# Optimization experiments

Hardware: AMD Instinct MI355X
Metric: run time of the kernel (lower is better)

The kernel has to match this reference:

```python
import jax, jax.numpy as jnp
import numpy as np

HEAD_DIM = 64
CLIP = 64  # clipping_distance
B, S = 32, 1024


def setup_inputs() -> dict:
    key = jax.random.key(0)
    kq, kk, kv, km, kt = jax.random.split(key, 5)
    q = jax.random.normal(kq, (B, S, HEAD_DIM), dtype=jnp.float32)
    k = jax.random.normal(kk, (B, S, HEAD_DIM), dtype=jnp.float32)
    v = jax.random.normal(kv, (B, S, HEAD_DIM), dtype=jnp.float32)
    mask = jax.random.randint(km, (B, S, S), 0, 2).astype(jnp.bool_)
    pos_table = jax.random.normal(kt, (2 * CLIP + 1, HEAD_DIM), dtype=jnp.float32)
    return {"q": q, "k": k, "v": v, "mask": mask, "pos_table": pos_table}


def reference(q, k, v, mask, pos_table):
    scaling = 1.0 / np.sqrt(HEAD_DIM).astype(np.float32)
    Sq, Sk = q.shape[1], k.shape[1]
    # relative positions k_idx - q_idx, clipped to [-CLIP, CLIP]
    rel = jnp.arange(Sk)[None, :] - jnp.arange(Sq)[:, None]      # [Sq, Sk]
    idx = jnp.clip(rel, -CLIP, CLIP) + CLIP                      # [Sq, Sk]
    pe = pos_table[idx]                                          # [Sq, Sk, D]
    # content logits + relative positional logits
    logits = jnp.einsum('bqd,bkd->bqk', q, k) + jnp.einsum('bqd,qkd->bqk', q, pe)
    logits = logits * scaling
    logits = jnp.where(mask, -jnp.inf, logits)
    attn = jax.nn.softmax(logits, axis=-1)                       # [B, Sq, Sk]
    return jnp.einsum('bqk,bkd->bqd', attn, v)
```

## Files before the change

### kernel.cpp

```cpp
#include <hip/hip_runtime.h>
#include <stdint.h>

#define BATCH 32
#define SEQ   1024
#define DIM   64
#define NKT   (SEQ / 64)

typedef uint8_t  u8;
typedef uint16_t u16;
typedef uint32_t u32;
typedef unsigned long long u64;
typedef __attribute__((ext_vector_type(8))) __bf16 bf16x8;
typedef __attribute__((ext_vector_type(4))) float  f32x4;
typedef __attribute__((ext_vector_type(4))) u32    u32x4;

__device__ __forceinline__ float fexp2(float x) {
#if __has_builtin(__builtin_amdgcn_exp2f)
    return __builtin_amdgcn_exp2f(x);
#else
    return exp2f(x);
#endif
}

__device__ __forceinline__ u16 f2bf(float f) {
    u32 x = __builtin_bit_cast(u32, f);
    x += 0x7FFFu + ((x >> 16) & 1u);
    return (u16)(x >> 16);
}

__device__ __forceinline__ bf16x8 cvt8(const float* __restrict__ p) {
    f32x4 a = *reinterpret_cast<const f32x4*>(p);
    f32x4 b = *reinterpret_cast<const f32x4*>(p + 4);
    u16 t[8];
    t[0] = f2bf(a[0]); t[1] = f2bf(a[1]); t[2] = f2bf(a[2]); t[3] = f2bf(a[3]);
    t[4] = f2bf(b[0]); t[5] = f2bf(b[1]); t[6] = f2bf(b[2]); t[7] = f2bf(b[3]);
    return __builtin_bit_cast(bf16x8, *reinterpret_cast<u32x4*>(t));
}

__device__ __forceinline__ bf16x8 cvt8s(const float* __restrict__ p, float s) {
    f32x4 a = *reinterpret_cast<const f32x4*>(p);
    f32x4 b = *reinterpret_cast<const f32x4*>(p + 4);
    u16 t[8];
    t[0] = f2bf(a[0] * s); t[1] = f2bf(a[1] * s); t[2] = f2bf(a[2] * s); t[3] = f2bf(a[3] * s);
    t[4] = f2bf(b[0] * s); t[5] = f2bf(b[1] * s); t[6] = f2bf(b[2] * s); t[7] = f2bf(b[3] * s);
    return __builtin_bit_cast(bf16x8, *reinterpret_cast<u32x4*>(t));
}

__device__ __forceinline__ bf16x8 ldg8(const u16* p) {
    u32x4 u = *reinterpret_cast<const u32x4*>(p);
    return __builtin_bit_cast(bf16x8, u);
}

__device__ __forceinline__ u32 pack4(u32x4 a) {
    return (u32)(a[0] != 0) | ((u32)(a[1] != 0) << 8) |
           ((u32)(a[2] != 0) << 16) | ((u32)(a[3] != 0) << 24);
}

__global__ __launch_bounds__(256) void prep_kv(
    const float* __restrict__ kg, const float* __restrict__ vg,
    u16* __restrict__ kb, u16* __restrict__ vtb_) {
    __shared__ u16 tile[64][72];
    const int t  = threadIdx.x;
    const int b  = blockIdx.x >> 4;
    const int k0 = (blockIdx.x & 15) * 64;

    {
        int kk = t >> 2;
        int d0 = (t & 3) * 16;
        const float* src = kg + ((size_t)b * SEQ + k0 + kk) * DIM + d0;
        u16 tmp[16];
#pragma unroll
        for (int i = 0; i < 4; ++i) {
            f32x4 a = *reinterpret_cast<const f32x4*>(src + i * 4);
            tmp[i * 4 + 0] = f2bf(a[0]); tmp[i * 4 + 1] = f2bf(a[1]);
            tmp[i * 4 + 2] = f2bf(a[2]); tmp[i * 4 + 3] = f2bf(a[3]);
        }
        u16* dst = kb + ((size_t)b * SEQ + k0 + kk) * DIM + d0;
        *reinterpret_cast<u32x4*>(dst)     = *reinterpret_cast<u32x4*>(tmp);
        *reinterpret_cast<u32x4*>(dst + 8) = *reinterpret_cast<u32x4*>(tmp + 8);
    }
    {
        const float* vb = vg + (size_t)b * SEQ * DIM;
        int kk = t >> 2;
        int d0 = (t & 3) * 16;
        const float* src = vb + (size_t)(k0 + kk) * DIM + d0;
        u16 tmp[16];
#pragma unroll
        for (int i = 0; i < 4; ++i) {
            f32x4 a = *reinterpret_cast<const f32x4*>(src + i * 4);
            tmp[i * 4 + 0] = f2bf(a[0]); tmp[i * 4 + 1] = f2bf(a[1]);
            tmp[i * 4 + 2] = f2bf(a[2]); tmp[i * 4 + 3] = f2bf(a[3]);
        }
        *reinterpret_cast<u32x4*>(&tile[kk][d0])     = *reinterpret_cast<u32x4*>(tmp);
        *reinterpret_cast<u32x4*>(&tile[kk][d0 + 8]) = *reinterpret_cast<u32x4*>(tmp + 8);
    }
    __syncthreads();
    u16* vtb = vtb_ + (size_t)b * DIM * SEQ;
#pragma unroll
    for (int i = 0; i < 2; ++i) {
        int d  = t / 8 + i * 32;
        int ks = (t % 8) * 8;
        u16 tmp[8];
#pragma unroll
        for (int j = 0; j < 8; ++j) tmp[j] = tile[ks + j][d];
        *reinterpret_cast<u32x4*>(vtb + (size_t)d * SEQ + k0 + ks) =
            *reinterpret_cast<u32x4*>(tmp);
    }
}

__global__ __launch_bounds__(512, 2) void attn_fast9(
    const float* __restrict__ qg, const u16* __restrict__ kbf,
    const u16* __restrict__ vt, const int* __restrict__ maskg,
    const float* __restrict__ ptg, float* __restrict__ outg) {
    __shared__ float qp[64][132];
    __shared__ u16   plds[8][16][72];
    __shared__ u8    mlds[8][16][64];

    const int b    = blockIdx.y;
    const int q0   = blockIdx.x * 64;
    const int tid  = threadIdx.x;
    const int wave = tid >> 6;
    const int lane = tid & 63;
    const int wq   = wave & 3;
    const int wk   = wave >> 2;
    const int quad = lane >> 4;
    const int c16  = lane & 15;

    const float SC = 0.125f * 1.44269504088896340736f;

    const float* qb = qg + ((size_t)b * SEQ + q0) * DIM;

    const bf16x8 qA0 = cvt8s(qb + (size_t)(wq * 16 + c16) * DIM + quad * 8, SC);
    const bf16x8 qA1 = cvt8s(qb + (size_t)(wq * 16 + c16) * DIM + 32 + quad * 8, SC);

    {
        const int jt0 = wk ? 5 : 0, jt1 = wk ? 9 : 5;
        for (int jt = jt0; jt < jt1; ++jt) {
            int j0 = jt * 16;
            int jr = min(j0 + c16, 128);
            bf16x8 b0 = cvt8(ptg + (size_t)jr * DIM + quad * 8);
            bf16x8 b1 = cvt8(ptg + (size_t)jr * DIM + 32 + quad * 8);
            f32x4 acc = {0.f, 0.f, 0.f, 0.f};
            acc = __builtin_amdgcn_mfma_f32_16x16x32_bf16(qA0, b0, acc, 0, 0, 0);
            acc = __builtin_amdgcn_mfma_f32_16x16x32_bf16(qA1, b1, acc, 0, 0, 0);
            int jcol = j0 + c16;
            if (jcol <= 128) {
#pragma unroll
                for (int r = 0; r < 4; ++r)
                    qp[wq * 16 + quad * 4 + r][jcol] = acc[r];
            }
        }
    }
    __syncthreads();

    float cL[4], cR[4];
#pragma unroll
    for (int r = 0; r < 4; ++r) {
        cL[r] = qp[wq * 16 + quad * 4 + r][0];
        cR[r] = qp[wq * 16 + quad * 4 + r][128];
    }

    const u16* kb_base  = kbf + (size_t)b * SEQ * DIM;
    const u16* vtb_base = vt  + (size_t)b * DIM * SEQ;
    const int  row_min  = q0 + wq * 16;
    const int  ktbase   = wk * 8;

    const int* mrow = maskg + ((size_t)b * SEQ + q0 + wq * 16 + (lane >> 2)) * SEQ +
                      (lane & 3) * 16;

    u32x4 mreg[2][4];
#pragma unroll
    for (int s = 0; s < 2; ++s) {
        const int* p = mrow + (size_t)(ktbase + s) * 64;
        mreg[s][0] = *reinterpret_cast<const u32x4*>(p);
        mreg[s][1] = *reinterpret_cast<const u32x4*>(p + 4);
        mreg[s][2] = *reinterpret_cast<const u32x4*>(p + 8);
        mreg[s][3] = *reinterpret_cast<const u32x4*>(p + 12);
    }

    bf16x8 kc0[4], kc1[4];
#pragma unroll
    for (int sub = 0; sub < 4; ++sub) {
        const u16* kr = kb_base + (size_t)(ktbase * 64 + sub * 16 + c16) * DIM;
        kc0[sub] = ldg8(kr + quad * 8);
        kc1[sub] = ldg8(kr + 32 + quad * 8);
    }

    float l_part[4];
    f32x4 O[4];
#pragma unroll
    for (int r = 0; r < 4; ++r) l_part[r] = 0.f;
#pragma unroll
    for (int d = 0; d < 4; ++d) O[d] = f32x4{0.f, 0.f, 0.f, 0.f};

#pragma unroll
    for (int j = 0; j < 8; ++j) {
        const int kt = ktbase + j;
        const int k0 = kt * 64;
        const int ms = j & 1;

        {
            u32x4 pk;
            pk[0] = pack4(mreg[ms][0]); pk[1] = pack4(mreg[ms][1]);
            pk[2] = pack4(mreg[ms][2]); pk[3] = pack4(mreg[ms][3]);
            *reinterpret_cast<u32x4*>(&mlds[wave][lane >> 2][(lane & 3) * 16]) = pk;
        }
        {
            const int* p = mrow + (size_t)((kt + 2) & 15) * 64;
            mreg[ms][0] = *reinterpret_cast<const u32x4*>(p);
            mreg[ms][1] = *reinterpret_cast<const u32x4*>(p + 4);
            mreg[ms][2] = *reinterpret_cast<const u32x4*>(p + 8);
            mreg[ms][3] = *reinterpret_cast<const u32x4*>(p + 12);
        }

        f32x4 S[4];
        __builtin_amdgcn_s_setprio(1);
#pragma unroll
        for (int sub = 0; sub < 4; ++sub) {
            f32x4 acc = {0.f, 0.f, 0.f, 0.f};
            acc = __builtin_amdgcn_mfma_f32_16x16x32_bf16(qA0, kc0[sub], acc, 0, 0, 0);
            acc = __builtin_amdgcn_mfma_f32_16x16x32_bf16(qA1, kc1[sub], acc, 0, 0, 0);
            S[sub] = acc;
        }
        __builtin_amdgcn_s_setprio(0);

        {
            const int kn = (ktbase + ((j + 1) & 7)) * 64;
#pragma unroll
            for (int sub = 0; sub < 4; ++sub) {
                const u16* kr = kb_base + (size_t)(kn + sub * 16 + c16) * DIM;
                kc0[sub] = ldg8(kr + quad * 8);
                kc1[sub] = ldg8(kr + 32 + quad * 8);
            }
        }

        bf16x8 vf0[4], vf1[4];
#pragma unroll
        for (int d = 0; d < 4; ++d) {
            const u16* vr = vtb_base + (size_t)(d * 16 + c16) * SEQ + k0;
            vf0[d] = ldg8(vr + quad * 8);
            vf1[d] = ldg8(vr + 32 + quad * 8);
        }

        const bool farL = (k0 + 127 <= row_min);
        const bool farR = (k0 >= row_min + 79);

        if (farL | farR) {
#pragma unroll
            for (int r = 0; r < 4; ++r) {
                const int row_l = quad * 4 + r;
                const float c = farL ? cL[r] : cR[r];
                float rs = 0.f;
#pragma unroll
                for (int sub = 0; sub < 4; ++sub) {
                    u8 mv = mlds[wave][row_l][sub * 16 + c16];
                    float e = mv ? 0.f : fexp2(S[sub][r] + c);
                    rs += e;
                    plds[wave][row_l][sub * 16 + c16] = f2bf(e);
                }
                l_part[r] += rs;
            }
        } else {
#pragma unroll
            for (int r = 0; r < 4; ++r) {
                const int row_l = quad * 4 + r;
                const int row_g = row_min + row_l;
                float rs = 0.f;
#pragma unroll
                for (int sub = 0; sub < 4; ++sub) {
                    int col_g = k0 + sub * 16 + c16;
                    int rel = col_g - row_g;
                    rel = rel < -64 ? -64 : (rel > 64 ? 64 : rel);
                    float x = S[sub][r] + qp[wq * 16 + row_l][rel + 64];
                    u8 mv = mlds[wave][row_l][sub * 16 + c16];
                    float e = mv ? 0.f : fexp2(x);
                    rs += e;
                    plds[wave][row_l][sub * 16 + c16] = f2bf(e);
                }
                l_part[r] += rs;
            }
        }

        bf16x8 pA0 = *reinterpret_cast<bf16x8*>(&plds[wave][c16][quad * 8]);
        bf16x8 pA1 = *reinterpret_cast<bf16x8*>(&plds[wave][c16][32 + quad * 8]);
        __builtin_amdgcn_s_setprio(1);
#pragma unroll
        for (int d = 0; d < 4; ++d) {
            O[d] = __builtin_amdgcn_mfma_f32_16x16x32_bf16(pA0, vf0[d], O[d], 0, 0, 0);
            O[d] = __builtin_amdgcn_mfma_f32_16x16x32_bf16(pA1, vf1[d], O[d], 0, 0, 0);
        }
        __builtin_amdgcn_s_setprio(0);
    }

    float l_run[4];
#pragma unroll
    for (int r = 0; r < 4; ++r) {
        float rs = l_part[r];
        rs += __shfl_xor(rs, 1);
        rs += __shfl_xor(rs, 2);
        rs += __shfl_xor(rs, 4);
        rs += __shfl_xor(rs, 8);
        l_run[r] = rs;
    }

    __syncthreads();
    float* cmb = &qp[0][0];
    const int cbase = (wq * 64 + lane) * 24;
    if (wk == 1) {
#pragma unroll
        for (int r = 0; r < 4; ++r) cmb[cbase + r] = l_run[r];
#pragma unroll
        for (int d = 0; d < 4; ++d)
#pragma unroll
            for (int r = 0; r < 4; ++r)
                cmb[cbase + 4 + d * 4 + r] = O[d][r];
    }
    __syncthreads();
    if (wk == 0) {
        float* ob = outg + ((size_t)b * SEQ + q0) * DIM;
#pragma unroll
        for (int r = 0; r < 4; ++r) {
            float inv = 1.f / (l_run[r] + cmb[cbase + r]);
            int row_l = wq * 16 + quad * 4 + r;
#pragma unroll
            for (int d = 0; d < 4; ++d) {
                float o = O[d][r] + cmb[cbase + 4 + d * 4 + r];
                ob[(size_t)row_l * DIM + d * 16 + c16] = o * inv;
            }
        }
    }
}

__global__ __launch_bounds__(256) void vt_kernel(const float* __restrict__ v,
                                                 u16* __restrict__ vt) {
    __shared__ u16 tile[64][72];
    const int b  = blockIdx.y;
    const int k0 = blockIdx.x * 64;
    const int t  = threadIdx.x;
    const float* vb  = v  + (size_t)b * SEQ * DIM;
    u16*         vtb = vt + (size_t)b * DIM * SEQ;

    {
        int kk = t >> 2;
        int d0 = (t & 3) * 16;
        const float* src = vb + (size_t)(k0 + kk) * DIM + d0;
        u16 tmp[16];
#pragma unroll
        for (int i = 0; i < 4; ++i) {
            f32x4 a = *reinterpret_cast<const f32x4*>(src + i * 4);
            tmp[i * 4 + 0] = f2bf(a[0]); tmp[i * 4 + 1] = f2bf(a[1]);
            tmp[i * 4 + 2] = f2bf(a[2]); tmp[i * 4 + 3] = f2bf(a[3]);
        }
        *reinterpret_cast<u32x4*>(&tile[kk][d0])     = *reinterpret_cast<u32x4*>(tmp);
        *reinterpret_cast<u32x4*>(&tile[kk][d0 + 8]) = *reinterpret_cast<u32x4*>(tmp + 8);
    }
    __syncthreads();
#pragma unroll
    for (int i = 0; i < 2; ++i) {
        int d  = t / 8 + i * 32;
        int ks = (t % 8) * 8;
        u16 tmp[8];
#pragma unroll
        for (int j = 0; j < 8; ++j) tmp[j] = tile[ks + j][d];
        *reinterpret_cast<u32x4*>(vtb + (size_t)d * SEQ + k0 + ks) =
            *reinterpret_cast<u32x4*>(tmp);
    }
}

template <bool USE_VT>
__global__ __launch_bounds__(256, 2) void attn_kernel(
    const float* __restrict__ qg, const float* __restrict__ kg,
    const void* __restrict__ vgv, const int* __restrict__ maskg,
    const float* __restrict__ ptg, float* __restrict__ outg) {
    __shared__ float qp[64][132];
    __shared__ int   mlds[4][16][68];
    __shared__ u16   plds[4][16][72];

    const int b    = blockIdx.y;
    const int q0   = blockIdx.x * 64;
    const int tid  = threadIdx.x;
    const int wave = tid >> 6;
    const int lane = tid & 63;
    const int quad = lane >> 4;
    const int c16  = lane & 15;

    const float* qb = qg + ((size_t)b * SEQ + q0) * DIM;
    const float* kb = kg + (size_t)b * SEQ * DIM;
    const int*   mb = maskg + ((size_t)b * SEQ + q0) * SEQ;

    const bf16x8 qA0 = cvt8(qb + (size_t)(wave * 16 + c16) * DIM + quad * 8);
    const bf16x8 qA1 = cvt8(qb + (size_t)(wave * 16 + c16) * DIM + 32 + quad * 8);

    for (int jt = 0; jt < 9; ++jt) {
        int j0 = jt * 16;
        int jr = min(j0 + c16, 128);
        bf16x8 b0 = cvt8(ptg + (size_t)jr * DIM + quad * 8);
        bf16x8 b1 = cvt8(ptg + (size_t)jr * DIM + 32 + quad * 8);
        f32x4 acc = {0.f, 0.f, 0.f, 0.f};
        acc = __builtin_amdgcn_mfma_f32_16x16x32_bf16(qA0, b0, acc, 0, 0, 0);
        acc = __builtin_amdgcn_mfma_f32_16x16x32_bf16(qA1, b1, acc, 0, 0, 0);
        int jcol = j0 + c16;
        if (jcol <= 128) {
#pragma unroll
            for (int r = 0; r < 4; ++r)
                qp[wave * 16 + quad * 4 + r][jcol] = acc[r];
        }
    }

    float m_run[4], l_run[4];
    f32x4 O[4];
#pragma unroll
    for (int r = 0; r < 4; ++r) { m_run[r] = -1e30f; l_run[r] = 0.f; }
#pragma unroll
    for (int d = 0; d < 4; ++d) O[d] = f32x4{0.f, 0.f, 0.f, 0.f};

#pragma unroll 1
    for (int kt = 0; kt < NKT; ++kt) {
        const int k0 = kt * 64;
        {
            int row_l = lane >> 2;
            const int* mrow = mb + (size_t)(wave * 16 + row_l) * SEQ + k0;
#pragma unroll
            for (int i = 0; i < 4; ++i) {
                int seg = (lane & 3) + i * 4;
                *reinterpret_cast<u32x4*>(&mlds[wave][row_l][seg * 4]) =
                    *reinterpret_cast<const u32x4*>(mrow + seg * 4);
            }
        }

        f32x4 S[4];
#pragma unroll
        for (int sub = 0; sub < 4; ++sub) {
            const float* kr = kb + (size_t)(k0 + sub * 16 + c16) * DIM;
            bf16x8 kb0 = cvt8(kr + quad * 8);
            bf16x8 kb1 = cvt8(kr + 32 + quad * 8);
            f32x4 acc = {0.f, 0.f, 0.f, 0.f};
            acc = __builtin_amdgcn_mfma_f32_16x16x32_bf16(qA0, kb0, acc, 0, 0, 0);
            acc = __builtin_amdgcn_mfma_f32_16x16x32_bf16(qA1, kb1, acc, 0, 0, 0);
            S[sub] = acc;
        }

        float sv[4][4];
#pragma unroll
        for (int sub = 0; sub < 4; ++sub) {
#pragma unroll
            for (int r = 0; r < 4; ++r) {
                int row_l = quad * 4 + r;
                int row_g = q0 + wave * 16 + row_l;
                int col_g = k0 + sub * 16 + c16;
                int rel = col_g - row_g;
                rel = rel < -64 ? -64 : (rel > 64 ? 64 : rel);
                float x = (S[sub][r] + qp[wave * 16 + row_l][rel + 64]) * 0.125f;
                int mv = mlds[wave][row_l][sub * 16 + c16];
                sv[sub][r] = mv ? -1e30f : x;
            }
        }

        float m_new[4], alpha[4];
#pragma unroll
        for (int r = 0; r < 4; ++r) {
            float rmax = fmaxf(fmaxf(sv[0][r], sv[1][r]), fmaxf(sv[2][r], sv[3][r]));
            rmax = fmaxf(rmax, __shfl_xor(rmax, 1));
            rmax = fmaxf(rmax, __shfl_xor(rmax, 2));
            rmax = fmaxf(rmax, __shfl_xor(rmax, 4));
            rmax = fmaxf(rmax, __shfl_xor(rmax, 8));
            m_new[r] = fmaxf(m_run[r], rmax);
            alpha[r] = __expf(m_run[r] - m_new[r]);
            m_run[r] = m_new[r];
        }
#pragma unroll
        for (int r = 0; r < 4; ++r) {
            float rs = 0.f;
#pragma unroll
            for (int sub = 0; sub < 4; ++sub) {
                float e = __expf(sv[sub][r] - m_new[r]);
                rs += e;
                plds[wave][quad * 4 + r][sub * 16 + c16] = f2bf(e);
            }
            rs += __shfl_xor(rs, 1);
            rs += __shfl_xor(rs, 2);
            rs += __shfl_xor(rs, 4);
            rs += __shfl_xor(rs, 8);
            l_run[r] = l_run[r] * alpha[r] + rs;
#pragma unroll
            for (int d = 0; d < 4; ++d) O[d][r] *= alpha[r];
        }

        bf16x8 pA0 = *reinterpret_cast<bf16x8*>(&plds[wave][c16][quad * 8]);
        bf16x8 pA1 = *reinterpret_cast<bf16x8*>(&plds[wave][c16][32 + quad * 8]);
#pragma unroll
        for (int d = 0; d < 4; ++d) {
            bf16x8 vb0, vb1;
            if (USE_VT) {
                const u16* vtb = (const u16*)vgv + (size_t)b * DIM * SEQ +
                                 (size_t)(d * 16 + c16) * SEQ + k0;
                vb0 = ldg8(vtb + quad * 8);
                vb1 = ldg8(vtb + 32 + quad * 8);
            } else {
                u16 t0[8], t1[8];
                const float* vbase = (const float*)vgv +
                                     ((size_t)b * SEQ + k0) * DIM + d * 16 + c16;
#pragma unroll
                for (int jj = 0; jj < 8; ++jj) {
                    t0[jj] = f2bf(vbase[(size_t)(quad * 8 + jj) * DIM]);
                    t1[jj] = f2bf(vbase[(size_t)(32 + quad * 8 + jj) * DIM]);
                }
                vb0 = __builtin_bit_cast(bf16x8, *reinterpret_cast<u32x4*>(t0));
                vb1 = __builtin_bit_cast(bf16x8, *reinterpret_cast<u32x4*>(t1));
            }
            O[d] = __builtin_amdgcn_mfma_f32_16x16x32_bf16(pA0, vb0, O[d], 0, 0, 0);
            O[d] = __builtin_amdgcn_mfma_f32_16x16x32_bf16(pA1, vb1, O[d], 0, 0, 0);
        }
    }

    float* ob = outg + ((size_t)b * SEQ + q0) * DIM;
#pragma unroll
    for (int r = 0; r < 4; ++r) {
        float inv = 1.f / l_run[r];
        int row_l = wave * 16 + quad * 4 + r;
#pragma unroll
        for (int d = 0; d < 4; ++d)
            ob[(size_t)row_l * DIM + d * 16 + c16] = O[d][r] * inv;
    }
}

extern "C" void kernel_launch(void* const* d_in, const int* in_sizes, int n_in,
                              void* d_out, int out_size, void* d_ws, size_t ws_size,
                              hipStream_t stream) {
    const float* q    = (const float*)d_in[0];
    const float* k    = (const float*)d_in[1];
    const float* v    = (const float*)d_in[2];
    const int*   mask = (const int*)d_in[3];
    const float* pt   = (const float*)d_in[4];
    float* out        = (float*)d_out;

    const size_t vt_bytes = (size_t)BATCH * SEQ * DIM * sizeof(u16);
    const size_t kb_bytes = (size_t)BATCH * SEQ * DIM * sizeof(u16);
    dim3 grid(SEQ / 64, BATCH);

    if (ws_size >= vt_bytes + kb_bytes) {
        u16* vt = (u16*)d_ws;
        u16* kb = (u16*)((char*)d_ws + vt_bytes);
        prep_kv<<<dim3(512), 256, 0, stream>>>(k, v, kb, vt);
        attn_fast9<<<grid, 512, 0, stream>>>(q, kb, vt, mask, pt, out);
    } else if (ws_size >= vt_bytes) {
        u16* vt = (u16*)d_ws;
        vt_kernel<<<grid, 256, 0, stream>>>(v, vt);
        attn_kernel<true><<<grid, 256, 0, stream>>>(q, k, (const void*)vt, mask, pt, out);
    } else {
        attn_kernel<false><<<grid, 256, 0, stream>>>(q, k, (const void*)v, mask, pt, out);
    }
}
```

Baseline: 258.3 us.

## Preload mask into per-lane bitmasks in MFMA layout, drop LDS mask staging

Instead of loading mask rows as vectors per iteration, packing them to bytes and staging through LDS, each lane loads up front exactly the 128 mask entries it needs in MFMA accumulator layout and packs them into eight 32-bit registers. The inner loop then tests bits instead of reading LDS. This removes the LDS writes and reads and the in-loop packing, but the loads become scalar 4-byte gathers with stride 16 elements. They are issued all at once before compute rather than prefetched two tiles ahead, so the mask traffic is less coalesced and less overlapped with MFMA work.

Measured after the change: 280.7 us. +8.7%, slower.

```diff
diff --git a/kernel.cpp b/kernel.cpp
--- a/kernel.cpp
+++ b/kernel.cpp
@@ -51,11 +51,6 @@
     return __builtin_bit_cast(bf16x8, u);
 }
 
-__device__ __forceinline__ u32 pack4(u32x4 a) {
-    return (u32)(a[0] != 0) | ((u32)(a[1] != 0) << 8) |
-           ((u32)(a[2] != 0) << 16) | ((u32)(a[3] != 0) << 24);
-}
-
 __global__ __launch_bounds__(256) void prep_kv(
     const float* __restrict__ kg, const float* __restrict__ vg,
     u16* __restrict__ kb, u16* __restrict__ vtb_) {
@@ -108,13 +103,12 @@
     }
 }
 
-__global__ __launch_bounds__(512, 2) void attn_fast9(
+__global__ __launch_bounds__(512, 2) void attn_fast10(
     const float* __restrict__ qg, const u16* __restrict__ kbf,
     const u16* __restrict__ vt, const int* __restrict__ maskg,
     const float* __restrict__ ptg, float* __restrict__ outg) {
     __shared__ float qp[64][132];
     __shared__ u16   plds[8][16][72];
-    __shared__ u8    mlds[8][16][64];
 
     const int b    = blockIdx.y;
     const int q0   = blockIdx.x * 64;
@@ -128,7 +122,27 @@
 
     const float SC = 0.125f * 1.44269504088896340736f;
 
-    const float* qb = qg + ((size_t)b * SEQ + q0) * DIM;
+    const float* qb     = qg + ((size_t)b * SEQ + q0) * DIM;
+    const int    ktbase = wk * 8;
+
+    u32 mbits[8];
+    {
+        const int* mb0 = maskg + ((size_t)b * SEQ + q0 + wq * 16 + quad * 4) * SEQ + c16;
+#pragma unroll
+        for (int t = 0; t < 8; ++t) {
+            const int col0 = (ktbase + t) * 64;
+            u32 bits = 0;
+#pragma unroll
+            for (int r = 0; r < 4; ++r) {
+#pragma unroll
+                for (int sub = 0; sub < 4; ++sub) {
+                    int v = mb0[(size_t)r * SEQ + col0 + sub * 16];
+                    bits |= (u32)(v != 0) << (r * 4 + sub);
+                }
+            }
+            mbits[t] = bits;
+        }
+    }
 
     const bf16x8 qA0 = cvt8s(qb + (size_t)(wq * 16 + c16) * DIM + quad * 8, SC);
     const bf16x8 qA1 = cvt8s(qb + (size_t)(wq * 16 + c16) * DIM + 32 + quad * 8, SC);
@@ -163,20 +177,6 @@
     const u16* kb_base  = kbf + (size_t)b * SEQ * DIM;
     const u16* vtb_base = vt  + (size_t)b * DIM * SEQ;
     const int  row_min  = q0 + wq * 16;
-    const int  ktbase   = wk * 8;
-
-    const int* mrow = maskg + ((size_t)b * SEQ + q0 + wq * 16 + (lane >> 2)) * SEQ +
-                      (lane & 3) * 16;
-
-    u32x4 mreg[2][4];
-#pragma unroll
-    for (int s = 0; s < 2; ++s) {
-        const int* p = mrow + (size_t)(ktbase + s) * 64;
-        mreg[s][0] = *reinterpret_cast<const u32x4*>(p);
-        mreg[s][1] = *reinterpret_cast<const u32x4*>(p + 4);
-        mreg[s][2] = *reinterpret_cast<const u32x4*>(p + 8);
-        mreg[s][3] = *reinterpret_cast<const u32x4*>(p + 12);
-    }
 
     bf16x8 kc0[4], kc1[4];
 #pragma unroll
@@ -197,21 +197,7 @@
     for (int j = 0; j < 8; ++j) {
         const int kt = ktbase + j;
         const int k0 = kt * 64;
-        const int ms = j & 1;
-
-        {
-            u32x4 pk;
-            pk[0] = pack4(mreg[ms][0]); pk[1] = pack4(mreg[ms][1]);
-            pk[2] = pack4(mreg[ms][2]); pk[3] = pack4(mreg[ms][3]);
-            *reinterpret_cast<u32x4*>(&mlds[wave][lane >> 2][(lane & 3) * 16]) = pk;
-        }
-        {
-            const int* p = mrow + (size_t)((kt + 2) & 15) * 64;
-            mreg[ms][0] = *reinterpret_cast<const u32x4*>(p);
-            mreg[ms][1] = *reinterpret_cast<const u32x4*>(p + 4);
-            mreg[ms][2] = *reinterpret_cast<const u32x4*>(p + 8);
-            mreg[ms][3] = *reinterpret_cast<const u32x4*>(p + 12);
-        }
+        const u32 bt = mbits[j];
 
         f32x4 S[4];
         __builtin_amdgcn_s_setprio(1);
@@ -253,7 +239,7 @@
                 float rs = 0.f;
 #pragma unroll
                 for (int sub = 0; sub < 4; ++sub) {
-                    u8 mv = mlds[wave][row_l][sub * 16 + c16];
+                    u32 mv = (bt >> (r * 4 + sub)) & 1u;
                     float e = mv ? 0.f : fexp2(S[sub][r] + c);
                     rs += e;
                     plds[wave][row_l][sub * 16 + c16] = f2bf(e);
@@ -272,7 +258,7 @@
                     int rel = col_g - row_g;
                     rel = rel < -64 ? -64 : (rel > 64 ? 64 : rel);
                     float x = S[sub][r] + qp[wq * 16 + row_l][rel + 64];
-                    u8 mv = mlds[wave][row_l][sub * 16 + c16];
+                    u32 mv = (bt >> (r * 4 + sub)) & 1u;
                     float e = mv ? 0.f : fexp2(x);
                     rs += e;
                     plds[wave][row_l][sub * 16 + c16] = f2bf(e);
@@ -542,7 +528,7 @@
         u16* vt = (u16*)d_ws;
         u16* kb = (u16*)((char*)d_ws + vt_bytes);
         prep_kv<<<dim3(512), 256, 0, stream>>>(k, v, kb, vt);
-        attn_fast9<<<grid, 512, 0, stream>>>(q, kb, vt, mask, pt, out);
+        attn_fast10<<<grid, 512, 0, stream>>>(q, kb, vt, mask, pt, out);
     } else if (ws_size >= vt_bytes) {
         u16* vt = (u16*)d_ws;
         vt_kernel<<<grid, 256, 0, stream>>>(v, vt);
```
